# Optimization experiments

Measured on AMD Instinct MI355X. Metric: run time of the kernel, lower is better.

Reference implementation:

```python
import jax, jax.numpy as jnp
import numpy as np

B, H, W = 16, 128, 128
CIN, HID, OUT = 1, 64, 1
WS, NH = 8, 4  # window size, num heads
HD = HID // NH  # head dim = 16


def setup_inputs() -> dict:
    key = jax.random.key(0)
    ks = jax.random.split(key, 32)
    s = 0.05
    d = {"x": jax.random.normal(ks[0], (B, H, W, CIN), jnp.float32)}
    ins = [CIN, HID]
    for l in range(2):
        cin = ins[l]
        kb = 1 + 7 * l
        d[f"conv_w{l}"] = jax.random.normal(ks[kb], (4 * HID, cin + HID, 3, 3), jnp.float32) * s
        d[f"conv_b{l}"] = jnp.zeros((4 * HID,), jnp.float32)
        d[f"px_w{l}"] = jax.random.normal(ks[kb + 1], (HID, cin, 3, 3), jnp.float32) * s
        d[f"py_w{l}"] = jax.random.normal(ks[kb + 2], (HID, cin, 3, 3), jnp.float32) * s
        d[f"qkv_w{l}"] = jax.random.normal(ks[kb + 3], (3 * HID, HID), jnp.float32) * s
        d[f"proj_w{l}"] = jax.random.normal(ks[kb + 4], (HID, HID), jnp.float32) * s
        d[f"proj_b{l}"] = jnp.zeros((HID,), jnp.float32)
    d["out_w"] = jax.random.normal(ks[20], (OUT, HID, 1, 1), jnp.float32) * s
    d["out_b"] = jnp.zeros((OUT,), jnp.float32)
    return d


def _conv(x, w, pad, b=None):
    y = jax.lax.conv_general_dilated(
        x, w, (1, 1), [(pad, pad), (pad, pad)],
        dimension_numbers=("NCHW", "OIHW", "NCHW"))
    if b is not None:
        y = y + b[None, :, None, None]
    return y


def _win_attn(x, qkv_w, proj_w, proj_b):
    # x: [B, H, W, C], H and W are multiples of WS (pad branch is a no-op)
    Bx, Hx, Wx, C = x.shape
    nw_h, nw_w = Hx // WS, Wx // WS
    xw = x.reshape(Bx, nw_h, WS, nw_w, WS, C).transpose(0, 1, 3, 2, 4, 5)
    xw = xw.reshape(-1, WS * WS, C)  # [N, T, C], N = B*nw_h*nw_w, T = 64
    qkv = (xw @ qkv_w.T).reshape(-1, WS * WS, 3, NH, HD).transpose(2, 0, 3, 1, 4)
    q, k, v = qkv[0], qkv[1], qkv[2]  # [N, NH, T, HD]
    attn = jax.nn.softmax(jnp.einsum("nhqd,nhkd->nhqk", q, k) * (HD ** -0.5), axis=-1)
    o = jnp.einsum("nhqk,nhkd->nhqd", attn, v).transpose(0, 2, 1, 3).reshape(-1, WS * WS, C)
    o = o @ proj_w.T + proj_b
    o = o.reshape(Bx, nw_h, nw_w, WS, WS, C).transpose(0, 1, 3, 2, 4, 5)
    return o.reshape(Bx, Hx, Wx, C)


def _cell(x, h, c, cw, cb, pxw, pyw, qw, pw, pb):
    # x: [B, Cin, H, W]; h, c: [B, HID, H, W]
    cc = _conv(jnp.concatenate([x, h], axis=1), cw, 1, cb)
    ci, cf, co, cg = jnp.split(cc, 4, axis=1)
    px = _conv(x, pxw, 1)
    py = _conv(x, pyw, 1)
    i = jax.nn.sigmoid(ci + px)
    f = jax.nn.sigmoid(cf + px)
    o = jax.nn.sigmoid(co + py)
    g = jnp.tanh(cg + py)
    c2 = f * c + i * g
    h2 = o * jnp.tanh(c2)
    h2 = _win_attn(h2.transpose(0, 2, 3, 1), qw, pw, pb).transpose(0, 3, 1, 2)
    return h2, c2


def reference(x, conv_w0, conv_b0, px_w0, py_w0, qkv_w0, proj_w0, proj_b0,
              conv_w1, conv_b1, px_w1, py_w1, qkv_w1, proj_w1, proj_b1,
              out_w, out_b):
    # 4D input path: [B,H,W,C] -> NCHW frame, seq_len = 1
    xin = x.transpose(0, 3, 1, 2)
    z = jnp.zeros((B, HID, H, W), x.dtype)
    h0, _ = _cell(xin, z, z, conv_w0, conv_b0, px_w0, py_w0, qkv_w0, proj_w0, proj_b0)
    h1, _ = _cell(h0, z, z, conv_w1, conv_b1, px_w1, py_w1, qkv_w1, proj_w1, proj_b1)
    out = _conv(h1, out_w, 0, out_b)  # 1x1 output conv on last layer's (T=1) output
    return out.transpose(0, 2, 3, 1)  # [B, H, W, OUT]
```

## Files before the change

### kernel.cpp

```cpp
#include <hip/hip_runtime.h>


#define DEVFN __device__ __forceinline__

typedef __attribute__((ext_vector_type(8))) short short8;
typedef __attribute__((ext_vector_type(4))) float f32x4;

DEVFN float sigmoidf_(float z) { return 1.0f / (1.0f + __expf(-z)); }

DEVFN float tanhf_(float x) {
    float e = __expf(2.0f * x);
    return 1.0f - 2.0f / (e + 1.0f);
}

DEVFN unsigned short f2bf(float f) {
    unsigned int u = __builtin_bit_cast(unsigned int, f);
    u += 0x7fffu + ((u >> 16) & 1u);
    return (unsigned short)(u >> 16);
}

DEVFN unsigned pkbf(float a, float b) {
    return (unsigned)f2bf(a) | ((unsigned)f2bf(b) << 16);
}

__global__ __launch_bounds__(256) void repack_kernel(
    const float* __restrict__ cw0, const float* __restrict__ pxw0, const float* __restrict__ pyw0,
    const float* __restrict__ cw1, const float* __restrict__ pxw1, const float* __restrict__ pyw1,
    const float* __restrict__ qkvw0, const float* __restrict__ projw0,
    const float* __restrict__ qkvw1, const float* __restrict__ projw1,
    unsigned short* __restrict__ pwc, float* __restrict__ pw0,
    unsigned short* __restrict__ qb0, unsigned short* __restrict__ pjb0,
    unsigned short* __restrict__ qb1, unsigned short* __restrict__ pjb1)
{
    int idx = blockIdx.x * 256 + threadIdx.x;
    if (idx < 184320) {
        int j = idx & 7;
        int lane = (idx >> 3) & 63;
        int ng = (idx >> 9) & 3;
        int t = idx >> 11;
        int kk = t % 18, g = t / 18;
        int c = ng * 16 + (lane & 15);
        int kcol = kk * 32 + (lane >> 4) * 8 + j;
        int pos = kcol >> 6, cin = kcol & 63;
        float v;
        if (g == 0)      v = cw1[((c      ) * 128 + cin) * 9 + pos];
        else if (g == 1) v = cw1[((128 + c) * 128 + cin) * 9 + pos];
        else if (g == 2) v = cw1[((192 + c) * 128 + cin) * 9 + pos];
        else if (g == 3) v = pxw1[(c * 64 + cin) * 9 + pos];
        else             v = pyw1[(c * 64 + cin) * 9 + pos];
        pwc[idx] = f2bf(v);
    } else if (idx < 187200) {
        int i2 = idx - 184320;
        int g = i2 / (9 * 64);
        int rem = i2 - g * (9 * 64);
        int pos = rem >> 6, c = rem & 63;
        float v;
        if (g == 0)      v = cw0[(c      ) * 585 + pos];
        else if (g == 1) v = cw0[(128 + c) * 585 + pos];
        else if (g == 2) v = cw0[(192 + c) * 585 + pos];
        else if (g == 3) v = pxw0[c * 9 + pos];
        else             v = pyw0[c * 9 + pos];
        pw0[i2] = v;
    } else if (idx < 187200 + 12288) {
        int i = idx - 187200;           qb0[i] = f2bf(qkvw0[i]);
    } else if (idx < 187200 + 24576) {
        int i = idx - 187200 - 12288;   qb1[i] = f2bf(qkvw1[i]);
    } else if (idx < 187200 + 24576 + 4096) {
        int i = idx - 187200 - 24576;   pjb0[i] = f2bf(projw0[i]);
    } else if (idx < 187200 + 24576 + 8192) {
        int i = idx - 187200 - 28672;   pjb1[i] = f2bf(projw1[i]);
    }
}

__global__ __launch_bounds__(256) void gates1_kernel(
    const float* __restrict__ x, const float* __restrict__ pw,
    const float* __restrict__ cb, unsigned short* __restrict__ dst)
{
    const int idx = blockIdx.x * 256 + threadIdx.x;
    const int pix = idx >> 4, ch0 = (idx & 15) * 4;
    const int b = pix >> 14, y = (pix >> 7) & 127, xq = pix & 127;

    float a[9];
#pragma unroll
    for (int dy = 0; dy < 3; ++dy)
#pragma unroll
        for (int dx = 0; dx < 3; ++dx) {
            int gy = y + dy - 1, gx = xq + dx - 1;
            a[dy * 3 + dx] = ((unsigned)gy < 128u && (unsigned)gx < 128u)
                ? x[(b * 128 + gy) * 128 + gx] : 0.f;
        }

    float acc[5][4];
#pragma unroll
    for (int g = 0; g < 5; ++g)
#pragma unroll
        for (int u = 0; u < 4; ++u) acc[g][u] = 0.f;

#pragma unroll
    for (int pos = 0; pos < 9; ++pos) {
        const float av = a[pos];
#pragma unroll
        for (int g = 0; g < 5; ++g) {
            const float4 w4 = *(const float4*)(pw + (g * 9 + pos) * 64 + ch0);
            acc[g][0] = fmaf(av, w4.x, acc[g][0]);
            acc[g][1] = fmaf(av, w4.y, acc[g][1]);
            acc[g][2] = fmaf(av, w4.z, acc[g][2]);
            acc[g][3] = fmaf(av, w4.w, acc[g][3]);
        }
    }

    float hv[4];
#pragma unroll
    for (int u = 0; u < 4; ++u) {
        float ci = acc[0][u] + cb[ch0 + u];
        float co = acc[1][u] + cb[128 + ch0 + u];
        float cg = acc[2][u] + cb[192 + ch0 + u];
        float iv = sigmoidf_(ci + acc[3][u]);
        float ov = sigmoidf_(co + acc[4][u]);
        float gv = tanhf_(cg + acc[4][u]);
        hv[u] = ov * tanhf_(iv * gv);
    }
    uint2 o;
    o.x = pkbf(hv[0], hv[1]);
    o.y = pkbf(hv[2], hv[3]);
    *(uint2*)(dst + (size_t)pix * 64 + ch0) = o;
}

__global__ __launch_bounds__(512, 2) void gates64_kernel(
    const unsigned short* __restrict__ src, const unsigned short* __restrict__ wtc,
    const float* __restrict__ cb, unsigned short* __restrict__ dst)
{
    __shared__ unsigned short lds[3 * 130 * 64];
    char* const sbase = (char*)lds;

    const int tid = threadIdx.x;
    const int bid = blockIdx.x;
    const int y = bid & 127, b = bid >> 7;

    for (int i4 = tid; i4 < 3 * 130 * 8; i4 += 512) {
        int r = i4 / (130 * 8);
        int rem = i4 - r * (130 * 8);
        int xx = rem >> 3, c8 = rem & 7;
        int gy = y + r - 1, gx = xx - 1;
        uint4 wv = make_uint4(0, 0, 0, 0);
        if ((unsigned)gy < 128u && (unsigned)gx < 128u)
            wv = *(const uint4*)(src + (((size_t)(b * 128 + gy) * 128 + gx) * 64 + c8 * 8));
        int addr = ((r * 130 + xx) * 128 + c8 * 16) ^ ((xx & 7) << 4);
        *(uint4*)(sbase + addr) = wv;
    }
    __syncthreads();

    const int lane = tid & 63;
    const int wv_ = tid >> 6;
    const int mg = wv_ >> 2;
    const int ng = wv_ & 3;
    const int r0 = lane & 15;
    const int hi = lane >> 4;
    const int wch = ng * 16 + r0;

    const unsigned short* wbase = wtc + (size_t)(ng * 64 + lane) * 8;

    f32x4 acc[4][5];
#pragma unroll
    for (int mt = 0; mt < 4; ++mt)
#pragma unroll
        for (int g = 0; g < 5; ++g) acc[mt][g] = (f32x4){0.f, 0.f, 0.f, 0.f};

#pragma unroll
    for (int kk = 0; kk < 18; ++kk) {
        const int pos = kk >> 1, dy = pos / 3, dx = pos % 3, chalf = kk & 1;
        const int swz = (((r0 + dx) & 7) << 4);
        short8 bfr[5];
#pragma unroll
        for (int g = 0; g < 5; ++g)
            bfr[g] = *(const short8*)(wbase + (g * 18 + kk) * 2048);
        short8 afr[4];
#pragma unroll
        for (int mt = 0; mt < 4; ++mt) {
            const int row = dy * 130 + mg * 64 + mt * 16 + r0 + dx;
            const int addr = (row * 128 + chalf * 64 + hi * 16) ^ swz;
            afr[mt] = *(const short8*)(sbase + addr);
        }
#pragma unroll
        for (int mt = 0; mt < 4; ++mt)
#pragma unroll
            for (int g = 0; g < 5; ++g)
                acc[mt][g] = __builtin_amdgcn_mfma_f32_16x16x32_bf16(
                    afr[mt], bfr[g], acc[mt][g], 0, 0, 0);
    }

    const float bci = cb[wch], bco = cb[128 + wch], bcg = cb[192 + wch];
    const int rowbase = (b * 128 + y) * 128;
#pragma unroll
    for (int mt = 0; mt < 4; ++mt) {
#pragma unroll
        for (int rg = 0; rg < 4; ++rg) {
            const int px_i = mg * 64 + mt * 16 + hi * 4 + rg;
            float ci = acc[mt][0][rg] + bci;
            float co = acc[mt][1][rg] + bco;
            float cg = acc[mt][2][rg] + bcg;
            float pxv = acc[mt][3][rg];
            float pyv = acc[mt][4][rg];
            float iv = sigmoidf_(ci + pxv);
            float ov = sigmoidf_(co + pyv);
            float gv = tanhf_(cg + pyv);
            dst[(size_t)(rowbase + px_i) * 64 + wch] = f2bf(ov * tanhf_(iv * gv));
        }
    }
}

template <int FUSE>
__global__ __launch_bounds__(256, 3) void attn_kernel(
    const unsigned short* __restrict__ src,
    const unsigned short* __restrict__ qkvwb,
    const unsigned short* __restrict__ projwb,
    const float* __restrict__ projb,
    unsigned short* __restrict__ dst,
    const float* __restrict__ outw,
    const float* __restrict__ outb,
    float* __restrict__ out)
{
    __shared__ char sm[49152];
    char* const Xs = sm;
    char* const Xo = sm + 8192;
    char* const Qa = sm + 16384;
    char* const Ka = sm + 24576;
    char* const VT = sm + 32768;
    char* const Ps = sm + 40960;

    const int tid = threadIdx.x;
    const int lane = tid & 63;
    const int w = __builtin_amdgcn_readfirstlane(tid >> 6);
    const int lo = lane & 15, hi = lane >> 4;
    const int wid = blockIdx.x;
    const int b = wid >> 8, rem = wid & 255, wy = rem >> 4, wx = rem & 15;
    const int pixbase = (b * 128 + wy * 8) * 128 + wx * 8;

    {
        const int t = tid >> 2, c0 = (tid & 3) * 16;
        const int pix = pixbase + (t >> 3) * 128 + (t & 7);
        const uint4* sp = (const uint4*)(src + (size_t)pix * 64 + c0);
        uint4 w0 = sp[0], w1 = sp[1];
        const int a = t * 128 + c0 * 2, sz = (t & 7) << 4;
        *(uint4*)(Xs + (a ^ sz)) = w0;
        *(uint4*)(Xs + ((a + 16) ^ sz)) = w1;
    }
    __syncthreads();

    const int trow = w * 16 + lo;
    const int tswz = (lo & 7) << 4;

#pragma unroll
    for (int h = 0; h < 4; ++h) {
        f32x4 cq = {0.f, 0.f, 0.f, 0.f}, ck = cq, cv = cq;
#pragma unroll
        for (int ks = 0; ks < 2; ++ks) {
            const int koff = hi * 8 + ks * 32;
            short8 xb = *(const short8*)(Xs + ((trow * 128 + koff * 2) ^ tswz));
            short8 aq = *(const short8*)(qkvwb + (h * 16 + lo) * 64 + koff);
            short8 ak = *(const short8*)(qkvwb + (64 + h * 16 + lo) * 64 + koff);
            short8 bv = *(const short8*)(qkvwb + (128 + h * 16 + lo) * 64 + koff);
            cq = __builtin_amdgcn_mfma_f32_16x16x32_bf16(aq, xb, cq, 0, 0, 0);
            ck = __builtin_amdgcn_mfma_f32_16x16x32_bf16(ak, xb, ck, 0, 0, 0);
            cv = __builtin_amdgcn_mfma_f32_16x16x32_bf16(xb, bv, cv, 0, 0, 0);
        }
        uint2 qw, kw, vw;
        qw.x = pkbf(cq[0] * 0.125f, cq[1] * 0.125f);
        qw.y = pkbf(cq[2] * 0.125f, cq[3] * 0.125f);
        kw.x = pkbf(ck[0], ck[1]); kw.y = pkbf(ck[2], ck[3]);
        vw.x = pkbf(cv[0], cv[1]); vw.y = pkbf(cv[2], cv[3]);
        *(uint2*)(Qa + ((trow * 128 + (h * 16 + hi * 4) * 2) ^ tswz)) = qw;
        *(uint2*)(Ka + ((trow * 128 + (h * 16 + hi * 4) * 2) ^ tswz)) = kw;
        *(uint2*)(VT + (((h * 16 + lo) * 128 + (w * 16 + hi * 4) * 2) ^ ((lo & 7) << 4))) = vw;
    }
    __syncthreads();

#pragma unroll 1
    for (int h = 0; h < 4; ++h) {
        const int hb = h * 32;
        short8 bq = *(const short8*)(Qa + ((trow * 128 + hb + (hi & 1) * 16) ^ tswz));
        f32x4 st[4];
#pragma unroll
        for (int mt = 0; mt < 4; ++mt) {
            short8 ak2 = *(const short8*)(Ka + (((mt * 16 + lo) * 128 + hb + (hi & 1) * 16) ^ ((lo & 7) << 4)));
            f32x4 z = {0.f, 0.f, 0.f, 0.f};
            st[mt] = __builtin_amdgcn_mfma_f32_16x16x32_bf16(ak2, bq, z, 0, 0, 0);
        }
        float mx = -1e30f;
#pragma unroll
        for (int mt = 0; mt < 4; ++mt)
#pragma unroll
            for (int r = 0; r < 4; ++r) mx = fmaxf(mx, st[mt][r]);
        mx = fmaxf(mx, __shfl_xor(mx, 16));
        mx = fmaxf(mx, __shfl_xor(mx, 32));
        float pv[16];
        float sum = 0.f;
#pragma unroll
        for (int mt = 0; mt < 4; ++mt)
#pragma unroll
            for (int r = 0; r < 4; ++r) {
                float e = __expf(st[mt][r] - mx);
                pv[mt * 4 + r] = e;
                sum += e;
            }
        sum += __shfl_xor(sum, 16);
        sum += __shfl_xor(sum, 32);
        const float rs = 1.0f / sum;
#pragma unroll
        for (int mt = 0; mt < 4; ++mt) {
            uint2 pw_;
            pw_.x = pkbf(pv[mt * 4 + 0] * rs, pv[mt * 4 + 1] * rs);
            pw_.y = pkbf(pv[mt * 4 + 2] * rs, pv[mt * 4 + 3] * rs);
            *(uint2*)(Ps + ((trow * 128 + (mt * 16 + hi * 4) * 2) ^ tswz)) = pw_;
        }
        f32x4 ot = {0.f, 0.f, 0.f, 0.f};
#pragma unroll
        for (int ks = 0; ks < 2; ++ks) {
            const int ko = (hi * 8 + ks * 32) * 2;
            short8 av = *(const short8*)(VT + (((h * 16 + lo) * 128 + ko) ^ ((lo & 7) << 4)));
            short8 bp = *(const short8*)(Ps + ((trow * 128 + ko) ^ tswz));
            ot = __builtin_amdgcn_mfma_f32_16x16x32_bf16(av, bp, ot, 0, 0, 0);
        }
        uint2 ow_;
        ow_.x = pkbf(ot[0], ot[1]); ow_.y = pkbf(ot[2], ot[3]);
        *(uint2*)(Xo + ((trow * 128 + (h * 16 + hi * 4) * 2) ^ tswz)) = ow_;
    }
    __syncthreads();

    f32x4 cy[4];
#pragma unroll
    for (int mt = 0; mt < 4; ++mt) cy[mt] = (f32x4){0.f, 0.f, 0.f, 0.f};
#pragma unroll
    for (int ks = 0; ks < 2; ++ks) {
        const int koff = hi * 8 + ks * 32;
        short8 bw = *(const short8*)(projwb + (w * 16 + lo) * 64 + koff);
#pragma unroll
        for (int mt = 0; mt < 4; ++mt) {
            short8 ax = *(const short8*)(Xo + (((mt * 16 + lo) * 128 + koff * 2) ^ ((lo & 7) << 4)));
            cy[mt] = __builtin_amdgcn_mfma_f32_16x16x32_bf16(ax, bw, cy[mt], 0, 0, 0);
        }
    }
    const float pb = projb[w * 16 + lo];

    if constexpr (FUSE == 0) {
#pragma unroll
        for (int mt = 0; mt < 4; ++mt) {
#pragma unroll
            for (int r = 0; r < 4; ++r) {
                const int tok = mt * 16 + hi * 4 + r;
                const int pix = pixbase + (tok >> 3) * 128 + (tok & 7);
                dst[(size_t)pix * 64 + w * 16 + lo] = f2bf(cy[mt][r] + pb);
            }
        }
    } else {
        const float owv = outw[w * 16 + lo];
        float* red = (float*)VT;
#pragma unroll
        for (int mt = 0; mt < 4; ++mt) {
#pragma unroll
            for (int r = 0; r < 4; ++r) {
                float s = (cy[mt][r] + pb) * owv;
                s += __shfl_xor(s, 1);
                s += __shfl_xor(s, 2);
                s += __shfl_xor(s, 4);
                s += __shfl_xor(s, 8);
                if (lo == 0) red[(mt * 16 + hi * 4 + r) * 4 + w] = s;
            }
        }
        __syncthreads();
        if (tid < 64) {
            const int tok = tid;
            float4 rv = *(const float4*)(red + tok * 4);
            const int pix = pixbase + (tok >> 3) * 128 + (tok & 7);
            out[pix] = (rv.x + rv.y) + (rv.z + rv.w) + outb[0];
        }
    }
}

extern "C" void kernel_launch(void* const* d_in, const int* in_sizes, int n_in,
                              void* d_out, int out_size, void* d_ws, size_t ws_size,
                              hipStream_t stream)
{
    const float* x      = (const float*)d_in[0];
    const float* cw0    = (const float*)d_in[1];
    const float* cb0    = (const float*)d_in[2];
    const float* pxw0   = (const float*)d_in[3];
    const float* pyw0   = (const float*)d_in[4];
    const float* qkvw0  = (const float*)d_in[5];
    const float* projw0 = (const float*)d_in[6];
    const float* projb0 = (const float*)d_in[7];
    const float* cw1    = (const float*)d_in[8];
    const float* cb1    = (const float*)d_in[9];
    const float* pxw1   = (const float*)d_in[10];
    const float* pyw1   = (const float*)d_in[11];
    const float* qkvw1  = (const float*)d_in[12];
    const float* projw1 = (const float*)d_in[13];
    const float* projb1 = (const float*)d_in[14];
    const float* outw   = (const float*)d_in[15];
    const float* outb   = (const float*)d_in[16];

    const size_t BUF = (size_t)16 * 128 * 128 * 64 * sizeof(float);
    char* ws = (char*)d_ws;
    unsigned short* bufA = (unsigned short*)ws;
    unsigned short* bufB = (unsigned short*)(ws + BUF);
    char* wsx = ws + 2 * BUF;
    unsigned short* pwc  = (unsigned short*)(wsx);
    float* pw0           = (float*)(wsx + 369664);
    unsigned short* qb0  = (unsigned short*)(wsx + 381440);
    unsigned short* pjb0 = (unsigned short*)(wsx + 406016);
    unsigned short* qb1  = (unsigned short*)(wsx + 414208);
    unsigned short* pjb1 = (unsigned short*)(wsx + 438784);

    repack_kernel<<<860, 256, 0, stream>>>(
        cw0, pxw0, pyw0, cw1, pxw1, pyw1,
        qkvw0, projw0, qkvw1, projw1,
        pwc, pw0, qb0, pjb0, qb1, pjb1);

    gates1_kernel<<<16384, 256, 0, stream>>>(x, pw0, cb0, bufA);
    attn_kernel<0><<<4096, 256, 0, stream>>>(bufA, qb0, pjb0, projb0, bufB,
                                             nullptr, nullptr, nullptr);
    gates64_kernel<<<2048, 512, 0, stream>>>(bufB, pwc, cb1, bufA);
    attn_kernel<1><<<4096, 256, 0, stream>>>(bufA, qb1, pjb1, projb1, nullptr,
                                             outw, outb, (float*)d_out);
}
```

Baseline: 346.2 us.

## Fuse layer-0 gate conv into first attention kernel; split gates64 into half-rows

The layer-0 gate computation (3x3 conv on the single-channel input plus LSTM nonlinearities) now runs inside the first attention kernel. Each window block loads a 10x10 input patch into shared memory and writes gate outputs directly into the attention tile, which removes a launch and the bf16 hidden-state round trip through global memory. Separately, the layer-1 gates kernel now uses 256-thread blocks covering half a row (64 pixels) instead of 512 threads covering a full row. That doubles the grid and shrinks shared memory per block, at the cost of reloading more halo columns. Each attention thread now holds 80 accumulators for the fused part, which raises register pressure.

```diff
diff --git a/kernel.cpp b/kernel.cpp
--- a/kernel.cpp
+++ b/kernel.cpp
@@ -72,93 +72,38 @@
     }
 }
 
-__global__ __launch_bounds__(256) void gates1_kernel(
-    const float* __restrict__ x, const float* __restrict__ pw,
-    const float* __restrict__ cb, unsigned short* __restrict__ dst)
-{
-    const int idx = blockIdx.x * 256 + threadIdx.x;
-    const int pix = idx >> 4, ch0 = (idx & 15) * 4;
-    const int b = pix >> 14, y = (pix >> 7) & 127, xq = pix & 127;
-
-    float a[9];
-#pragma unroll
-    for (int dy = 0; dy < 3; ++dy)
-#pragma unroll
-        for (int dx = 0; dx < 3; ++dx) {
-            int gy = y + dy - 1, gx = xq + dx - 1;
-            a[dy * 3 + dx] = ((unsigned)gy < 128u && (unsigned)gx < 128u)
-                ? x[(b * 128 + gy) * 128 + gx] : 0.f;
-        }
-
-    float acc[5][4];
-#pragma unroll
-    for (int g = 0; g < 5; ++g)
-#pragma unroll
-        for (int u = 0; u < 4; ++u) acc[g][u] = 0.f;
-
-#pragma unroll
-    for (int pos = 0; pos < 9; ++pos) {
-        const float av = a[pos];
-#pragma unroll
-        for (int g = 0; g < 5; ++g) {
-            const float4 w4 = *(const float4*)(pw + (g * 9 + pos) * 64 + ch0);
-            acc[g][0] = fmaf(av, w4.x, acc[g][0]);
-            acc[g][1] = fmaf(av, w4.y, acc[g][1]);
-            acc[g][2] = fmaf(av, w4.z, acc[g][2]);
-            acc[g][3] = fmaf(av, w4.w, acc[g][3]);
-        }
-    }
-
-    float hv[4];
-#pragma unroll
-    for (int u = 0; u < 4; ++u) {
-        float ci = acc[0][u] + cb[ch0 + u];
-        float co = acc[1][u] + cb[128 + ch0 + u];
-        float cg = acc[2][u] + cb[192 + ch0 + u];
-        float iv = sigmoidf_(ci + acc[3][u]);
-        float ov = sigmoidf_(co + acc[4][u]);
-        float gv = tanhf_(cg + acc[4][u]);
-        hv[u] = ov * tanhf_(iv * gv);
-    }
-    uint2 o;
-    o.x = pkbf(hv[0], hv[1]);
-    o.y = pkbf(hv[2], hv[3]);
-    *(uint2*)(dst + (size_t)pix * 64 + ch0) = o;
-}
-
-__global__ __launch_bounds__(512, 2) void gates64_kernel(
+__global__ __launch_bounds__(256, 2) void gates64_kernel(
     const unsigned short* __restrict__ src, const unsigned short* __restrict__ wtc,
     const float* __restrict__ cb, unsigned short* __restrict__ dst)
 {
-    __shared__ unsigned short lds[3 * 130 * 64];
+    __shared__ unsigned short lds[3 * 66 * 64];
     char* const sbase = (char*)lds;
 
     const int tid = threadIdx.x;
     const int bid = blockIdx.x;
-    const int y = bid & 127, b = bid >> 7;
-
-    for (int i4 = tid; i4 < 3 * 130 * 8; i4 += 512) {
-        int r = i4 / (130 * 8);
-        int rem = i4 - r * (130 * 8);
+    const int xt = bid & 1, y = (bid >> 1) & 127, b = bid >> 8;
+    const int x0 = xt * 64;
+
+    for (int i4 = tid; i4 < 3 * 66 * 8; i4 += 256) {
+        int r = i4 / (66 * 8);
+        int rem = i4 - r * (66 * 8);
         int xx = rem >> 3, c8 = rem & 7;
-        int gy = y + r - 1, gx = xx - 1;
+        int gy = y + r - 1, gx = x0 + xx - 1;
         uint4 wv = make_uint4(0, 0, 0, 0);
         if ((unsigned)gy < 128u && (unsigned)gx < 128u)
             wv = *(const uint4*)(src + (((size_t)(b * 128 + gy) * 128 + gx) * 64 + c8 * 8));
-        int addr = ((r * 130 + xx) * 128 + c8 * 16) ^ ((xx & 7) << 4);
+        int addr = ((r * 66 + xx) * 128 + c8 * 16) ^ ((xx & 7) << 4);
         *(uint4*)(sbase + addr) = wv;
     }
     __syncthreads();
 
     const int lane = tid & 63;
     const int wv_ = tid >> 6;
-    const int mg = wv_ >> 2;
-    const int ng = wv_ & 3;
     const int r0 = lane & 15;
     const int hi = lane >> 4;
-    const int wch = ng * 16 + r0;
-
-    const unsigned short* wbase = wtc + (size_t)(ng * 64 + lane) * 8;
+    const int wch = wv_ * 16 + r0;
+
+    const unsigned short* wbase = wtc + (size_t)(wv_ * 64 + lane) * 8;
 
     f32x4 acc[4][5];
 #pragma unroll
@@ -177,7 +122,7 @@
         short8 afr[4];
 #pragma unroll
         for (int mt = 0; mt < 4; ++mt) {
-            const int row = dy * 130 + mg * 64 + mt * 16 + r0 + dx;
+            const int row = dy * 66 + mt * 16 + r0 + dx;
             const int addr = (row * 128 + chalf * 64 + hi * 16) ^ swz;
             afr[mt] = *(const short8*)(sbase + addr);
         }
@@ -190,12 +135,12 @@
     }
 
     const float bci = cb[wch], bco = cb[128 + wch], bcg = cb[192 + wch];
-    const int rowbase = (b * 128 + y) * 128;
+    const int rowbase = (b * 128 + y) * 128 + x0;
 #pragma unroll
     for (int mt = 0; mt < 4; ++mt) {
 #pragma unroll
         for (int rg = 0; rg < 4; ++rg) {
-            const int px_i = mg * 64 + mt * 16 + hi * 4 + rg;
+            const int px_i = mt * 16 + hi * 4 + rg;
             float ci = acc[mt][0][rg] + bci;
             float co = acc[mt][1][rg] + bco;
             float cg = acc[mt][2][rg] + bcg;
@@ -209,8 +154,11 @@
     }
 }
 
-template <int FUSE>
+template <int MODE>
 __global__ __launch_bounds__(256, 3) void attn_kernel(
+    const float* __restrict__ xin,
+    const float* __restrict__ pw0g,
+    const float* __restrict__ cb0,
     const unsigned short* __restrict__ src,
     const unsigned short* __restrict__ qkvwb,
     const unsigned short* __restrict__ projwb,
@@ -236,7 +184,68 @@
     const int b = wid >> 8, rem = wid & 255, wy = rem >> 4, wx = rem & 15;
     const int pixbase = (b * 128 + wy * 8) * 128 + wx * 8;
 
-    {
+    if constexpr (MODE == 0) {
+        float* xpatch = (float*)Xo;
+        if (tid < 120) {
+            int r = tid / 12, c = tid % 12;
+            float v = 0.f;
+            int gy = wy * 8 + r - 1, gx = wx * 8 + c - 1;
+            if (c < 10 && (unsigned)gy < 128u && (unsigned)gx < 128u)
+                v = xin[(b * 128 + gy) * 128 + gx];
+            xpatch[tid] = v;
+        }
+        __syncthreads();
+
+        const int px_ = tid >> 2, ch0 = (tid & 3) * 16;
+        const int ty = px_ >> 3, tx = px_ & 7;
+        float a[9];
+#pragma unroll
+        for (int dy = 0; dy < 3; ++dy)
+#pragma unroll
+            for (int dx = 0; dx < 3; ++dx)
+                a[dy * 3 + dx] = xpatch[(ty + dy) * 12 + tx + dx];
+
+        float acc[5][16];
+#pragma unroll
+        for (int g = 0; g < 5; ++g)
+#pragma unroll
+            for (int u = 0; u < 16; ++u) acc[g][u] = 0.f;
+#pragma unroll
+        for (int pos = 0; pos < 9; ++pos) {
+            const float av = a[pos];
+#pragma unroll
+            for (int g = 0; g < 5; ++g) {
+#pragma unroll
+                for (int u4 = 0; u4 < 4; ++u4) {
+                    const float4 w4 = *(const float4*)(pw0g + (g * 9 + pos) * 64 + ch0 + 4 * u4);
+                    acc[g][4 * u4 + 0] = fmaf(av, w4.x, acc[g][4 * u4 + 0]);
+                    acc[g][4 * u4 + 1] = fmaf(av, w4.y, acc[g][4 * u4 + 1]);
+                    acc[g][4 * u4 + 2] = fmaf(av, w4.z, acc[g][4 * u4 + 2]);
+                    acc[g][4 * u4 + 3] = fmaf(av, w4.w, acc[g][4 * u4 + 3]);
+                }
+            }
+        }
+        float hv[16];
+#pragma unroll
+        for (int u = 0; u < 16; ++u) {
+            float ci = acc[0][u] + cb0[ch0 + u];
+            float co = acc[1][u] + cb0[128 + ch0 + u];
+            float cg = acc[2][u] + cb0[192 + ch0 + u];
+            float iv = sigmoidf_(ci + acc[3][u]);
+            float ov = sigmoidf_(co + acc[4][u]);
+            float gv = tanhf_(cg + acc[4][u]);
+            hv[u] = ov * tanhf_(iv * gv);
+        }
+        uint4 w0, w1;
+        w0.x = pkbf(hv[0], hv[1]);   w0.y = pkbf(hv[2], hv[3]);
+        w0.z = pkbf(hv[4], hv[5]);   w0.w = pkbf(hv[6], hv[7]);
+        w1.x = pkbf(hv[8], hv[9]);   w1.y = pkbf(hv[10], hv[11]);
+        w1.z = pkbf(hv[12], hv[13]); w1.w = pkbf(hv[14], hv[15]);
+        __syncthreads();
+        const int a_ = px_ * 128 + ch0 * 2, sz = (px_ & 7) << 4;
+        *(uint4*)(Xs + (a_ ^ sz)) = w0;
+        *(uint4*)(Xs + ((a_ + 16) ^ sz)) = w1;
+    } else {
         const int t = tid >> 2, c0 = (tid & 3) * 16;
         const int pix = pixbase + (t >> 3) * 128 + (t & 7);
         const uint4* sp = (const uint4*)(src + (size_t)pix * 64 + c0);
@@ -342,7 +351,7 @@
     }
     const float pb = projb[w * 16 + lo];
 
-    if constexpr (FUSE == 0) {
+    if constexpr (MODE == 0) {
 #pragma unroll
         for (int mt = 0; mt < 4; ++mt) {
 #pragma unroll
@@ -416,10 +425,11 @@
         qkvw0, projw0, qkvw1, projw1,
         pwc, pw0, qb0, pjb0, qb1, pjb1);
 
-    gates1_kernel<<<16384, 256, 0, stream>>>(x, pw0, cb0, bufA);
-    attn_kernel<0><<<4096, 256, 0, stream>>>(bufA, qb0, pjb0, projb0, bufB,
-                                             nullptr, nullptr, nullptr);
-    gates64_kernel<<<2048, 512, 0, stream>>>(bufB, pwc, cb1, bufA);
-    attn_kernel<1><<<4096, 256, 0, stream>>>(bufA, qb1, pjb1, projb1, nullptr,
-                                             outw, outb, (float*)d_out);
-}
+    attn_kernel<0><<<4096, 256, 0, stream>>>(
+        x, pw0, cb0, nullptr, qb0, pjb0, projb0, bufB,
+        nullptr, nullptr, nullptr);
+    gates64_kernel<<<4096, 256, 0, stream>>>(bufB, pwc, cb1, bufA);
+    attn_kernel<1><<<4096, 256, 0, stream>>>(
+        nullptr, nullptr, nullptr, bufA, qb1, pjb1, projb1, nullptr,
+        outw, outb, (float*)d_out);
+}
```

Result: slower. 406.7 us (median of 2 runs) (+17.5%).
